# Performance work log

Measured on AMD Instinct MI355X. Metric: run time of the kernel, lower is better.

Reference implementation:

```python
import jax, jax.numpy as jnp
import numpy as np

B, R, C, NH, G = 32, 64, 96, 3, 8   # batch, patches_resolution, dim, heads, group(window) size
HD = C // NH                         # head dim = 32
SCALE = HD ** -0.5
HID = 4 * C                          # mlp hidden = mlp_ratio * dim


def setup_inputs() -> dict:
    key = jax.random.key(0)
    ks = jax.random.split(key, 16)
    n = jax.random.normal
    s = 0.02
    return {
        "x": n(ks[0], (B, R * R, C), jnp.float32),
        "w_qkv": n(ks[1], (C, 3 * C), jnp.float32) * s,
        "b_qkv": jnp.zeros((3 * C,), jnp.float32),
        "w_lepe": n(ks[2], (C, 1, 3, 3), jnp.float32) * s,  # depthwise conv, OIHW with groups=C
        "b_lepe": jnp.zeros((C,), jnp.float32),
        "w_proj": n(ks[3], (C, C), jnp.float32) * s,
        "b_proj": jnp.zeros((C,), jnp.float32),
        "g1": jnp.ones((C,), jnp.float32),
        "bt1": jnp.zeros((C,), jnp.float32),
        "g2": jnp.ones((C,), jnp.float32),
        "bt2": jnp.zeros((C,), jnp.float32),
        "w_fc1": n(ks[4], (C, HID), jnp.float32) * s,
        "b_fc1": jnp.zeros((HID,), jnp.float32),
        "w_fc2": n(ks[5], (HID, C), jnp.float32) * s,
        "b_fc2": jnp.zeros((C,), jnp.float32),
    }


def _ln(x, g, b):
    m = x.mean(-1, keepdims=True)
    v = ((x - m) ** 2).mean(-1, keepdims=True)
    return (x - m) * jax.lax.rsqrt(v + 1e-5) * g + b


def reference(x, w_qkv, b_qkv, w_lepe, b_lepe, w_proj, b_proj,
              g1, bt1, g2, bt2, w_fc1, b_fc1, w_fc2, b_fc2):
    Bn, L, _ = x.shape
    H = W = R
    shortcut = x
    # norm1 + SDA window partition: (B,H,W,C) -> (B*nW, G*G, C)
    h = _ln(x, g1, bt1).reshape(Bn, H // G, G, W // G, G, C)
    h = h.transpose(0, 1, 3, 2, 4, 5).reshape(-1, G * G, C)
    B_ = h.shape[0]
    qkv = (h @ w_qkv + b_qkv).reshape(B_, G * G, 3, NH, HD).transpose(2, 0, 3, 1, 4)
    q, k, v = qkv[0], qkv[1], qkv[2]            # (B_, NH, G*G, HD)
    # LePE: depthwise 3x3 conv on V viewed as (B_, C, G, G)
    vimg = v.transpose(0, 1, 3, 2).reshape(B_, C, G, G)
    lepe = jax.lax.conv_general_dilated(
        vimg, w_lepe, window_strides=(1, 1), padding='SAME',
        feature_group_count=C, dimension_numbers=('NCHW', 'OIHW', 'NCHW'))
    lepe = lepe + b_lepe[None, :, None, None]
    lepe = lepe.reshape(B_, NH, HD, G * G).transpose(0, 1, 3, 2)  # (B_, NH, G*G, HD)
    # attention (no mask registered in this block)
    attn = jax.nn.softmax((q * SCALE) @ k.transpose(0, 1, 3, 2), axis=-1)
    o = (attn @ v + lepe).transpose(0, 2, 1, 3).reshape(B_, G * G, C)
    o = o @ w_proj + b_proj
    # window reverse
    o = o.reshape(Bn, H // G, W // G, G, G, C).transpose(0, 1, 3, 2, 4, 5).reshape(Bn, L, C)
    x1 = shortcut + o
    # MLP block (exact GELU, as torch nn.GELU default)
    m = _ln(x1, g2, bt2)
    m = jax.nn.gelu(m @ w_fc1 + b_fc1, approximate=False) @ w_fc2 + b_fc2
    return (x1 + m, attn)
```

## Files before the change

kernel.cpp:

```cpp
#include <hip/hip_runtime.h>
#include <hip/hip_bf16.h>

typedef short short8 __attribute__((ext_vector_type(8)));
typedef float f32x4 __attribute__((ext_vector_type(4)));

constexpr int BDIM = 32, RDIM = 64, CDIM = 96, NH_ = 3, HD_ = 32;
constexpr int LTOK = RDIM * RDIM;
constexpr int GG = 64;
constexpr int HID = 384;
constexpr int NWIN = 2048;
constexpr float SCALE = 0.17677669529663687f;
constexpr long OUT1OFF = (long)BDIM * LTOK * CDIM;

constexpr int O_WQKVT = 0;
constexpr int O_WPROJT = 27648;
constexpr int O_WFC1T = 36864;
constexpr int O_WFC2T = 73728;
constexpr int W_TOT = 110592;

__device__ __forceinline__ unsigned short f2b(float f) {
  return __builtin_bit_cast(unsigned short, __float2bfloat16(f));
}
__device__ __forceinline__ float b2f(unsigned short u) {
  return __bfloat162float(__builtin_bit_cast(__hip_bfloat16, u));
}

__global__ void prep_weights(const float* __restrict__ wqkv,
                             const float* __restrict__ wproj,
                             const float* __restrict__ wfc1,
                             const float* __restrict__ wfc2,
                             unsigned short* __restrict__ ws) {
  int i = blockIdx.x * 256 + threadIdx.x;
  if (i >= W_TOT) return;
  float v;
  if (i < O_WPROJT) {
    int n = i / 96, k = i - n * 96;
    v = wqkv[k * 288 + n];
  } else if (i < O_WFC1T) {
    int j = i - O_WPROJT, n = j / 96, k = j - n * 96;
    v = wproj[k * 96 + n];
  } else if (i < O_WFC2T) {
    int j = i - O_WFC1T, n = j / 96, k = j - n * 96;
    v = wfc1[k * 384 + n];
  } else {
    int j = i - O_WFC2T, n = j / 384, k = j - n * 384;
    v = wfc2[k * 96 + n];
  }
  ws[i] = f2b(v);
}

__global__ __launch_bounds__(256, 2)
void attn_mfma(const float* __restrict__ x, const float* __restrict__ bqkv,
               const float* __restrict__ wlepe, const float* __restrict__ blepe,
               const float* __restrict__ bproj, const float* __restrict__ g1,
               const float* __restrict__ bt1,
               const unsigned short* __restrict__ ws, float* __restrict__ out) {
  constexpr int SA = 104;
  constexpr int SQ = 200;
  constexpr int SV = 72;
  constexpr int SP = 72;
  __shared__ __attribute__((aligned(16))) unsigned short hA[64 * SA];
  __shared__ __attribute__((aligned(16))) unsigned short qkS[64 * SQ];
  __shared__ __attribute__((aligned(16))) unsigned short vS[96 * SV];
  __shared__ __attribute__((aligned(16))) unsigned short pS[64 * SP];
  float* red = (float*)pS;

  const int tid = threadIdx.x, lane = tid & 63;
  const int wv = __builtin_amdgcn_readfirstlane(tid >> 6);
  const int w = blockIdx.x, b = w >> 6, wi = w & 63, wr = wi >> 3, wc = wi & 7;
  const long xbase = (long)b * (LTOK * CDIM);
  const int l15 = lane & 15, lk = (lane >> 4) * 8, lr = (lane >> 4) * 4;

  {
    const int tok = lane;
    const long rowbase =
        xbase + (long)((wr * 8 + (tok >> 3)) * RDIM + wc * 8 + (tok & 7)) * CDIM;
    float xv[24], s1 = 0.f, s2 = 0.f;
#pragma unroll
    for (int i = 0; i < 24; ++i) {
      float v = x[rowbase + wv * 24 + i];
      xv[i] = v; s1 += v; s2 += v * v;
    }
    red[wv * 64 + tok] = s1;
    red[256 + wv * 64 + tok] = s2;
    __syncthreads();
    float m = 0.f, vv = 0.f;
#pragma unroll
    for (int q = 0; q < 4; ++q) { m += red[q * 64 + tok]; vv += red[256 + q * 64 + tok]; }
    m *= (1.f / 96.f);
    vv = vv * (1.f / 96.f) - m * m;
    float rs = rsqrtf(vv + 1e-5f);
#pragma unroll
    for (int i = 0; i < 24; ++i) {
      int c = wv * 24 + i;
      hA[tok * SA + c] = f2b((xv[i] - m) * rs * g1[c] + bt1[c]);
    }
  }
  __syncthreads();

  {
    f32x4 acc[18];
#pragma unroll
    for (int t = 0; t < 18; ++t) acc[t] = (f32x4){0.f, 0.f, 0.f, 0.f};
    const int arow = wv * 16 + l15;
#pragma unroll
    for (int kk = 0; kk < 3; ++kk) {
      short8 a = *(const short8*)&hA[arow * SA + kk * 32 + lk];
#pragma unroll
      for (int nt = 0; nt < 18; ++nt) {
        short8 bw = *(const short8*)&ws[O_WQKVT + (nt * 16 + l15) * 96 + kk * 32 + lk];
        acc[nt] = __builtin_amdgcn_mfma_f32_16x16x32_bf16(a, bw, acc[nt], 0, 0, 0);
      }
    }
#pragma unroll
    for (int nt = 0; nt < 18; ++nt) {
      int n0 = nt * 16 + l15;
      float bias = bqkv[n0];
#pragma unroll
      for (int r = 0; r < 4; ++r) {
        int tk = wv * 16 + lr + r;
        float v = acc[nt][r] + bias;
        if (n0 < 96) qkS[tk * SQ + n0] = f2b(v * SCALE);
        else if (n0 < 192) qkS[tk * SQ + n0] = f2b(v);
        else vS[(n0 - 192) * SV + tk] = f2b(v);
      }
    }
  }
  __syncthreads();

  for (int h = 0; h < NH_; ++h) {
    f32x4 sacc[4];
#pragma unroll
    for (int t = 0; t < 4; ++t) sacc[t] = (f32x4){0.f, 0.f, 0.f, 0.f};
    short8 aq = *(const short8*)&qkS[(wv * 16 + l15) * SQ + h * 32 + lk];
#pragma unroll
    for (int nt = 0; nt < 4; ++nt) {
      short8 bk = *(const short8*)&qkS[(nt * 16 + l15) * SQ + 96 + h * 32 + lk];
      sacc[nt] = __builtin_amdgcn_mfma_f32_16x16x32_bf16(aq, bk, sacc[nt], 0, 0, 0);
    }
    float p[4][4];
#pragma unroll
    for (int r = 0; r < 4; ++r) {
      float mx = -1e30f;
#pragma unroll
      for (int nt = 0; nt < 4; ++nt) mx = fmaxf(mx, sacc[nt][r]);
#pragma unroll
      for (int s = 1; s < 16; s <<= 1) mx = fmaxf(mx, __shfl_xor(mx, s, 64));
      float sum = 0.f;
#pragma unroll
      for (int nt = 0; nt < 4; ++nt) {
        float e = __expf(sacc[nt][r] - mx);
        p[nt][r] = e; sum += e;
      }
#pragma unroll
      for (int s = 1; s < 16; s <<= 1) sum += __shfl_xor(sum, s, 64);
      float inv = 1.f / sum;
#pragma unroll
      for (int nt = 0; nt < 4; ++nt) p[nt][r] *= inv;
    }
    const long o1base = OUT1OFF + ((long)(w * NH_ + h) * GG) * GG;
#pragma unroll
    for (int nt = 0; nt < 4; ++nt) {
      int col = nt * 16 + l15;
#pragma unroll
      for (int r = 0; r < 4; ++r) {
        int row = wv * 16 + lr + r;
        out[o1base + (long)row * GG + col] = p[nt][r];
        pS[row * SP + col] = f2b(p[nt][r]);
      }
    }
    f32x4 oa[2];
    oa[0] = (f32x4){0.f, 0.f, 0.f, 0.f};
    oa[1] = (f32x4){0.f, 0.f, 0.f, 0.f};
#pragma unroll
    for (int kk = 0; kk < 2; ++kk) {
      short8 ap = *(const short8*)&pS[(wv * 16 + l15) * SP + kk * 32 + lk];
#pragma unroll
      for (int nt = 0; nt < 2; ++nt) {
        short8 bv = *(const short8*)&vS[(h * 32 + nt * 16 + l15) * SV + kk * 32 + lk];
        oa[nt] = __builtin_amdgcn_mfma_f32_16x16x32_bf16(ap, bv, oa[nt], 0, 0, 0);
      }
    }
#pragma unroll
    for (int nt = 0; nt < 2; ++nt) {
      int d = nt * 16 + l15, c = h * 32 + d;
      float lw9[9];
#pragma unroll
      for (int q = 0; q < 9; ++q) lw9[q] = wlepe[c * 9 + q];
      float lb = blepe[c];
#pragma unroll
      for (int r = 0; r < 4; ++r) {
        int tk = wv * 16 + lr + r;
        int tr_ = tk >> 3, tc_ = tk & 7;
        float a = lb;
#pragma unroll
        for (int kh = 0; kh < 3; ++kh)
#pragma unroll
          for (int kw2 = 0; kw2 < 3; ++kw2) {
            int rr = tr_ + kh - 1, cc = tc_ + kw2 - 1;
            if (rr >= 0 && rr < 8 && cc >= 0 && cc < 8)
              a += lw9[kh * 3 + kw2] * b2f(vS[c * SV + rr * 8 + cc]);
          }
        hA[tk * SA + c] = f2b(oa[nt][r] + a);
      }
    }
  }
  __syncthreads();

  {
    f32x4 pacc[6];
#pragma unroll
    for (int t = 0; t < 6; ++t) pacc[t] = (f32x4){0.f, 0.f, 0.f, 0.f};
#pragma unroll
    for (int kk = 0; kk < 3; ++kk) {
      short8 ao = *(const short8*)&hA[(wv * 16 + l15) * SA + kk * 32 + lk];
#pragma unroll
      for (int nt = 0; nt < 6; ++nt) {
        short8 bw = *(const short8*)&ws[O_WPROJT + (nt * 16 + l15) * 96 + kk * 32 + lk];
        pacc[nt] = __builtin_amdgcn_mfma_f32_16x16x32_bf16(ao, bw, pacc[nt], 0, 0, 0);
      }
    }
#pragma unroll
    for (int nt = 0; nt < 6; ++nt) {
      int ch = nt * 16 + l15;
      float bias = bproj[ch];
#pragma unroll
      for (int r = 0; r < 4; ++r) {
        int tk = wv * 16 + lr + r;
        long g = xbase + (long)((wr * 8 + (tk >> 3)) * RDIM + wc * 8 + (tk & 7)) * CDIM + ch;
        out[g] = x[g] + pacc[nt][r] + bias;
      }
    }
  }
}

__global__ __launch_bounds__(256, 2)
void mlp_mfma(const float* __restrict__ bfc1, const float* __restrict__ bfc2,
              const float* __restrict__ g2, const float* __restrict__ bt2,
              const unsigned short* __restrict__ ws, float* __restrict__ out) {
  constexpr int SB = 104, SH = 392;
  __shared__ __attribute__((aligned(16))) unsigned short hB[64 * SB];
  __shared__ __attribute__((aligned(16))) unsigned short Hs[64 * SH];
  float* red = (float*)Hs;

  const int tid = threadIdx.x, lane = tid & 63;
  const int wv = __builtin_amdgcn_readfirstlane(tid >> 6);
  const long t0 = (long)blockIdx.x * GG;
  const int l15 = lane & 15, lk = (lane >> 4) * 8, lr = (lane >> 4) * 4;

  {
    const int tok = lane;
    const long rb = (t0 + tok) * CDIM;
    float xv[24], s1 = 0.f, s2 = 0.f;
#pragma unroll
    for (int i = 0; i < 24; ++i) {
      float v = out[rb + wv * 24 + i];
      xv[i] = v; s1 += v; s2 += v * v;
    }
    red[wv * 64 + tok] = s1;
    red[256 + wv * 64 + tok] = s2;
    __syncthreads();
    float m = 0.f, vv = 0.f;
#pragma unroll
    for (int q = 0; q < 4; ++q) { m += red[q * 64 + tok]; vv += red[256 + q * 64 + tok]; }
    m *= (1.f / 96.f);
    vv = vv * (1.f / 96.f) - m * m;
    float rs = rsqrtf(vv + 1e-5f);
#pragma unroll
    for (int i = 0; i < 24; ++i) {
      int c = wv * 24 + i;
      hB[tok * SB + c] = f2b((xv[i] - m) * rs * g2[c] + bt2[c]);
    }
  }
  __syncthreads();

  for (int half = 0; half < 2; ++half) {
    f32x4 acc[12];
#pragma unroll
    for (int t = 0; t < 12; ++t) acc[t] = (f32x4){0.f, 0.f, 0.f, 0.f};
#pragma unroll
    for (int kk = 0; kk < 3; ++kk) {
      short8 a = *(const short8*)&hB[(wv * 16 + l15) * SB + kk * 32 + lk];
#pragma unroll
      for (int nt = 0; nt < 12; ++nt) {
        int n = half * 192 + nt * 16 + l15;
        short8 bw = *(const short8*)&ws[O_WFC1T + n * 96 + kk * 32 + lk];
        acc[nt] = __builtin_amdgcn_mfma_f32_16x16x32_bf16(a, bw, acc[nt], 0, 0, 0);
      }
    }
#pragma unroll
    for (int nt = 0; nt < 12; ++nt) {
      int n = half * 192 + nt * 16 + l15;
      float bias = bfc1[n];
#pragma unroll
      for (int r = 0; r < 4; ++r) {
        int tk = wv * 16 + lr + r;
        float v = acc[nt][r] + bias;
        float gl = 0.5f * v * (1.f + erff(v * 0.70710678118654752f));
        Hs[tk * SH + n] = f2b(gl);
      }
    }
  }
  __syncthreads();

  {
    f32x4 acc[6];
#pragma unroll
    for (int t = 0; t < 6; ++t) acc[t] = (f32x4){0.f, 0.f, 0.f, 0.f};
#pragma unroll
    for (int kk = 0; kk < 12; ++kk) {
      short8 a = *(const short8*)&Hs[(wv * 16 + l15) * SH + kk * 32 + lk];
#pragma unroll
      for (int nt = 0; nt < 6; ++nt) {
        short8 bw = *(const short8*)&ws[O_WFC2T + (nt * 16 + l15) * 384 + kk * 32 + lk];
        acc[nt] = __builtin_amdgcn_mfma_f32_16x16x32_bf16(a, bw, acc[nt], 0, 0, 0);
      }
    }
#pragma unroll
    for (int nt = 0; nt < 6; ++nt) {
      int ch = nt * 16 + l15;
      float bias = bfc2[ch];
#pragma unroll
      for (int r = 0; r < 4; ++r) {
        int tk = wv * 16 + lr + r;
        long g = (t0 + tk) * CDIM + ch;
        out[g] = out[g] + acc[nt][r] + bias;
      }
    }
  }
}

struct PF {
  const float *x, *w_qkv, *b_qkv, *w_lepe, *b_lepe, *w_proj, *b_proj;
  const float *g1, *bt1, *g2, *bt2, *w_fc1, *b_fc1, *w_fc2, *b_fc2;
  float* out;
};

__global__ __launch_bounds__(256, 2)
void attn_scalar(PF p) {
  constexpr int SA = 66;
  __shared__ __hip_bfloat16 bufA[CDIM * SA];
  __shared__ __hip_bfloat16 qkvT[288 * GG];
  __shared__ __hip_bfloat16 sPad[GG * SA];
  __shared__ float meanS[GG], rstdS[GG];

  const int w = blockIdx.x;
  const int b = w >> 6, wi = w & 63, wr = wi >> 3, wc = wi & 7;
  const int tid = threadIdx.x, lane = tid & 63;
  const int wv = __builtin_amdgcn_readfirstlane(tid >> 6);
  const long xbase = (long)b * (LTOK * CDIM);

  for (int k = 0; k < 24; ++k) {
    int e = tid + k * 256, wrow = e / 768, o = e - wrow * 768;
    int tir = o / 96, ch = o - tir * 96;
    long g = xbase + ((wr * 8 + wrow) * RDIM + wc * 8 + tir) * CDIM + ch;
    bufA[ch * SA + wrow * 8 + tir] = __float2bfloat16(p.x[g]);
  }
  __syncthreads();
  if (wv == 0) {
    float m = 0.f;
    for (int c = 0; c < CDIM; ++c) m += __bfloat162float(bufA[c * SA + lane]);
    m *= (1.f / CDIM);
    float var = 0.f;
    for (int c = 0; c < CDIM; ++c) {
      float d = __bfloat162float(bufA[c * SA + lane]) - m;
      var += d * d;
    }
    meanS[lane] = m;
    rstdS[lane] = rsqrtf(var * (1.f / CDIM) + 1e-5f);
  }
  __syncthreads();
  {
    float m = meanS[lane], rs = rstdS[lane];
    for (int cc = 0; cc < 24; ++cc) {
      int c = wv * 24 + cc;
      float v = __bfloat162float(bufA[c * SA + lane]);
      bufA[c * SA + lane] = __float2bfloat16((v - m) * rs * p.g1[c] + p.bt1[c]);
    }
  }
  __syncthreads();
  for (int tile = 0; tile < 2; ++tile) {
    int j0 = wv * 72 + tile * 36;
    float acc[36];
#pragma unroll
    for (int jj = 0; jj < 36; ++jj) acc[jj] = p.b_qkv[j0 + jj];
#pragma unroll 1
    for (int c = 0; c < CDIM; ++c) {
      float hv = __bfloat162float(bufA[c * SA + lane]);
#pragma unroll
      for (int jj = 0; jj < 36; ++jj) acc[jj] += hv * p.w_qkv[c * 288 + j0 + jj];
    }
#pragma unroll
    for (int jj = 0; jj < 36; ++jj)
      qkvT[(j0 + jj) * GG + lane] = __float2bfloat16(acc[jj]);
  }
  __syncthreads();
  for (int hh = 0; hh < NH_; ++hh) {
    float kreg[HD_];
#pragma unroll
    for (int d = 0; d < HD_; ++d)
      kreg[d] = __bfloat162float(qkvT[(CDIM + hh * HD_ + d) * GG + lane]);
#pragma unroll 1
    for (int r = 0; r < 16; ++r) {
      int i = wv * 16 + r;
      float acc = 0.f;
#pragma unroll
      for (int d = 0; d < HD_; ++d)
        acc += __bfloat162float(qkvT[(hh * HD_ + d) * GG + i]) * kreg[d];
      sPad[lane * SA + i] = __float2bfloat16(acc * SCALE);
    }
#pragma unroll 1
    for (int r = 0; r < 16; ++r) {
      int i = wv * 16 + r;
      float v = __bfloat162float(sPad[lane * SA + i]);
      float mx = v;
#pragma unroll
      for (int s = 32; s > 0; s >>= 1) mx = fmaxf(mx, __shfl_xor(mx, s, 64));
      float e = __expf(v - mx);
      float sum = e;
#pragma unroll
      for (int s = 32; s > 0; s >>= 1) sum += __shfl_xor(sum, s, 64);
      float rr = e / sum;
      sPad[lane * SA + i] = __float2bfloat16(rr);
      p.out[OUT1OFF + ((long)(w * NH_ + hh) * GG + i) * GG + lane] = rr;
    }
    __syncthreads();
    {
      int d0 = wv * 8;
      float acc[8];
#pragma unroll
      for (int dd = 0; dd < 8; ++dd) acc[dd] = 0.f;
#pragma unroll 1
      for (int j = 0; j < GG; ++j) {
        float sv = __bfloat162float(sPad[j * SA + lane]);
#pragma unroll
        for (int dd = 0; dd < 8; ++dd)
          acc[dd] += sv * __bfloat162float(qkvT[(2 * CDIM + hh * HD_ + d0 + dd) * GG + j]);
      }
      int tr = lane >> 3, tc = lane & 7;
#pragma unroll
      for (int dd = 0; dd < 8; ++dd) {
        int c = hh * HD_ + d0 + dd;
        float a = p.b_lepe[c];
#pragma unroll
        for (int kh = 0; kh < 3; ++kh)
#pragma unroll
          for (int kw = 0; kw < 3; ++kw) {
            int rr2 = tr + kh - 1, cc2 = tc + kw - 1;
            if (rr2 >= 0 && rr2 < 8 && cc2 >= 0 && cc2 < 8)
              a += p.w_lepe[c * 9 + kh * 3 + kw] *
                   __bfloat162float(qkvT[(2 * CDIM + hh * HD_ + d0 + dd) * GG + rr2 * 8 + cc2]);
          }
        acc[dd] += a;
      }
#pragma unroll
      for (int dd = 0; dd < 8; ++dd)
        bufA[(hh * HD_ + d0 + dd) * SA + lane] = __float2bfloat16(acc[dd]);
    }
    __syncthreads();
  }
  __hip_bfloat16* projT = qkvT;
  {
    int j0 = wv * 24;
    float acc[24];
#pragma unroll
    for (int jj = 0; jj < 24; ++jj) acc[jj] = p.b_proj[j0 + jj];
#pragma unroll 1
    for (int c = 0; c < CDIM; ++c) {
      float ov = __bfloat162float(bufA[c * SA + lane]);
#pragma unroll
      for (int jj = 0; jj < 24; ++jj) acc[jj] += ov * p.w_proj[c * CDIM + j0 + jj];
    }
#pragma unroll
    for (int jj = 0; jj < 24; ++jj)
      projT[(j0 + jj) * SA + lane] = __float2bfloat16(acc[jj]);
  }
  __syncthreads();
  for (int k = 0; k < 24; ++k) {
    int e = tid + k * 256, wrow = e / 768, o = e - wrow * 768;
    int tir = o / 96, ch = o - tir * 96;
    long g = xbase + ((wr * 8 + wrow) * RDIM + wc * 8 + tir) * CDIM + ch;
    p.out[g] = p.x[g] + __bfloat162float(projT[ch * SA + wrow * 8 + tir]);
  }
}

__global__ __launch_bounds__(256, 2)
void mlp_scalar(PF p) {
  constexpr int SB = 66;
  __shared__ __hip_bfloat16 bufB[CDIM * SB];
  __shared__ __hip_bfloat16 hidT[HID * GG];
  __shared__ float meanS[GG], rstdS[GG];

  const int tid = threadIdx.x, lane = tid & 63;
  const int wv = __builtin_amdgcn_readfirstlane(tid >> 6);
  const long t0 = (long)blockIdx.x * GG;

  for (int k = 0; k < 24; ++k) {
    int e = tid + k * 256, tok = e / 96, ch = e - tok * 96;
    bufB[ch * SB + tok] = __float2bfloat16(p.out[(t0 + tok) * CDIM + ch]);
  }
  __syncthreads();
  if (wv == 0) {
    float m = 0.f;
    for (int c = 0; c < CDIM; ++c) m += __bfloat162float(bufB[c * SB + lane]);
    m *= (1.f / CDIM);
    float var = 0.f;
    for (int c = 0; c < CDIM; ++c) {
      float d = __bfloat162float(bufB[c * SB + lane]) - m;
      var += d * d;
    }
    meanS[lane] = m;
    rstdS[lane] = rsqrtf(var * (1.f / CDIM) + 1e-5f);
  }
  __syncthreads();
  {
    float m = meanS[lane], rs = rstdS[lane];
    for (int cc = 0; cc < 24; ++cc) {
      int c = wv * 24 + cc;
      float v = __bfloat162float(bufB[c * SB + lane]);
      bufB[c * SB + lane] = __float2bfloat16((v - m) * rs * p.g2[c] + p.bt2[c]);
    }
  }
  __syncthreads();
  for (int tile = 0; tile < 4; ++tile) {
    int j0 = wv * 96 + tile * 24;
    float acc[24];
#pragma unroll
    for (int jj = 0; jj < 24; ++jj) acc[jj] = p.b_fc1[j0 + jj];
#pragma unroll 1
    for (int c = 0; c < CDIM; ++c) {
      float hv = __bfloat162float(bufB[c * SB + lane]);
#pragma unroll
      for (int jj = 0; jj < 24; ++jj) acc[jj] += hv * p.w_fc1[c * HID + j0 + jj];
    }
#pragma unroll
    for (int jj = 0; jj < 24; ++jj) {
      float xg = acc[jj];
      hidT[(j0 + jj) * GG + lane] =
          __float2bfloat16(0.5f * xg * (1.f + erff(xg * 0.70710678118f)));
    }
  }
  __syncthreads();
  {
    int j0 = wv * 24;
    float acc[24];
#pragma unroll
    for (int jj = 0; jj < 24; ++jj) acc[jj] = p.b_fc2[j0 + jj];
#pragma unroll 1
    for (int h = 0; h < HID; ++h) {
      float hv = __bfloat162float(hidT[h * GG + lane]);
#pragma unroll
      for (int jj = 0; jj < 24; ++jj) acc[jj] += hv * p.w_fc2[h * CDIM + j0 + jj];
    }
#pragma unroll
    for (int jj = 0; jj < 24; ++jj)
      bufB[(j0 + jj) * SB + lane] = __float2bfloat16(acc[jj]);
  }
  __syncthreads();
  for (int k = 0; k < 24; ++k) {
    int e = tid + k * 256, tok = e / 96, ch = e - tok * 96;
    long g = (t0 + tok) * CDIM + ch;
    p.out[g] = p.out[g] + __bfloat162float(bufB[ch * SB + tok]);
  }
}

extern "C" void kernel_launch(void* const* d_in, const int* in_sizes, int n_in,
                              void* d_out, int out_size, void* d_ws, size_t ws_size,
                              hipStream_t stream) {
  const float* x = (const float*)d_in[0];
  const float* w_qkv = (const float*)d_in[1];
  const float* b_qkv = (const float*)d_in[2];
  const float* w_lepe = (const float*)d_in[3];
  const float* b_lepe = (const float*)d_in[4];
  const float* w_proj = (const float*)d_in[5];
  const float* b_proj = (const float*)d_in[6];
  const float* g1 = (const float*)d_in[7];
  const float* bt1 = (const float*)d_in[8];
  const float* g2 = (const float*)d_in[9];
  const float* bt2 = (const float*)d_in[10];
  const float* w_fc1 = (const float*)d_in[11];
  const float* b_fc1 = (const float*)d_in[12];
  const float* w_fc2 = (const float*)d_in[13];
  const float* b_fc2 = (const float*)d_in[14];
  float* out = (float*)d_out;
  const int mlp_blocks = (BDIM * LTOK) / GG;

  if (ws_size >= (size_t)W_TOT * sizeof(unsigned short)) {
    unsigned short* ws = (unsigned short*)d_ws;
    prep_weights<<<(W_TOT + 255) / 256, 256, 0, stream>>>(w_qkv, w_proj, w_fc1, w_fc2, ws);
    attn_mfma<<<NWIN, 256, 0, stream>>>(x, b_qkv, w_lepe, b_lepe, b_proj, g1, bt1, ws, out);
    mlp_mfma<<<mlp_blocks, 256, 0, stream>>>(b_fc1, b_fc2, g2, bt2, ws, out);
  } else {
    PF p{x, w_qkv, b_qkv, w_lepe, b_lepe, w_proj, b_proj,
         g1, bt1, g2, bt2, w_fc1, b_fc1, w_fc2, b_fc2, out};
    attn_scalar<<<NWIN, 256, 0, stream>>>(p);
    mlp_scalar<<<mlp_blocks, 256, 0, stream>>>(p);
  }
}
```

Before: 425.8 us.

## Fuse attention and MLP into one per-window kernel with head-streamed QKV

Merges the attention and MLP kernels into a single per-window kernel. The post-attention residual x1 stays in registers and LayerNorm2 is computed in-register via lane shuffles, so x1 is no longer written to and re-read from global memory. QKV is now computed per head and the projection is accumulated per head, and the MLP streams the hidden dimension in 64-wide chunks so fc2 accumulates without a full hidden buffer. Together these shrink LDS use enough to raise the occupancy hint from 2 to 4 blocks, at the cost of more barriers per window. The scalar fallback path is removed, so a workspace buffer is now assumed.

```diff
diff --git a/kernel.cpp b/kernel.cpp
--- a/kernel.cpp
+++ b/kernel.cpp
@@ -4,10 +4,9 @@
 typedef short short8 __attribute__((ext_vector_type(8)));
 typedef float f32x4 __attribute__((ext_vector_type(4)));
 
-constexpr int BDIM = 32, RDIM = 64, CDIM = 96, NH_ = 3, HD_ = 32;
+constexpr int BDIM = 32, RDIM = 64, CDIM = 96;
 constexpr int LTOK = RDIM * RDIM;
 constexpr int GG = 64;
-constexpr int HID = 384;
 constexpr int NWIN = 2048;
 constexpr float SCALE = 0.17677669529663687f;
 constexpr long OUT1OFF = (long)BDIM * LTOK * CDIM;
@@ -49,27 +48,31 @@
   ws[i] = f2b(v);
 }
 
-__global__ __launch_bounds__(256, 2)
-void attn_mfma(const float* __restrict__ x, const float* __restrict__ bqkv,
-               const float* __restrict__ wlepe, const float* __restrict__ blepe,
-               const float* __restrict__ bproj, const float* __restrict__ g1,
-               const float* __restrict__ bt1,
-               const unsigned short* __restrict__ ws, float* __restrict__ out) {
+__global__ __launch_bounds__(256, 4)
+void fused_block(const float* __restrict__ x, const float* __restrict__ bqkv,
+                 const float* __restrict__ wlepe, const float* __restrict__ blepe,
+                 const float* __restrict__ bproj, const float* __restrict__ g1,
+                 const float* __restrict__ bt1, const float* __restrict__ g2v,
+                 const float* __restrict__ bt2, const float* __restrict__ bfc1,
+                 const float* __restrict__ bfc2,
+                 const unsigned short* __restrict__ ws, float* __restrict__ out) {
   constexpr int SA = 104;
-  constexpr int SQ = 200;
+  constexpr int SQ = 72;
   constexpr int SV = 72;
   constexpr int SP = 72;
+  constexpr int SO = 32;
   __shared__ __attribute__((aligned(16))) unsigned short hA[64 * SA];
   __shared__ __attribute__((aligned(16))) unsigned short qkS[64 * SQ];
-  __shared__ __attribute__((aligned(16))) unsigned short vS[96 * SV];
+  __shared__ __attribute__((aligned(16))) unsigned short vS[32 * SV];
   __shared__ __attribute__((aligned(16))) unsigned short pS[64 * SP];
+  __shared__ __attribute__((aligned(16))) unsigned short oS[64 * SO];
   float* red = (float*)pS;
 
   const int tid = threadIdx.x, lane = tid & 63;
   const int wv = __builtin_amdgcn_readfirstlane(tid >> 6);
   const int w = blockIdx.x, b = w >> 6, wi = w & 63, wr = wi >> 3, wc = wi & 7;
   const long xbase = (long)b * (LTOK * CDIM);
-  const int l15 = lane & 15, lk = (lane >> 4) * 8, lr = (lane >> 4) * 4;
+  const int l15 = lane & 15, quad = lane >> 4, lk = quad * 8, lr = quad * 4;
 
   {
     const int tok = lane;
@@ -91,51 +94,67 @@
     vv = vv * (1.f / 96.f) - m * m;
     float rs = rsqrtf(vv + 1e-5f);
 #pragma unroll
-    for (int i = 0; i < 24; ++i) {
-      int c = wv * 24 + i;
-      hA[tok * SA + c] = f2b((xv[i] - m) * rs * g1[c] + bt1[c]);
+    for (int j = 0; j < 3; ++j) {
+      short8 hp;
+#pragma unroll
+      for (int e = 0; e < 8; ++e) {
+        int c = wv * 24 + j * 8 + e;
+        ((unsigned short*)&hp)[e] = f2b((xv[j * 8 + e] - m) * rs * g1[c] + bt1[c]);
+      }
+      *(short8*)&hA[lane * SA + wv * 24 + j * 8] = hp;
     }
   }
   __syncthreads();
 
-  {
-    f32x4 acc[18];
-#pragma unroll
-    for (int t = 0; t < 18; ++t) acc[t] = (f32x4){0.f, 0.f, 0.f, 0.f};
-    const int arow = wv * 16 + l15;
+  short8 Afrag[3];
+#pragma unroll
+  for (int kk = 0; kk < 3; ++kk)
+    Afrag[kk] = *(const short8*)&hA[(wv * 16 + l15) * SA + kk * 32 + lk];
+
+  f32x4 accP[6];
+#pragma unroll
+  for (int t = 0; t < 6; ++t) accP[t] = (f32x4){0.f, 0.f, 0.f, 0.f};
+
+#pragma unroll 1
+  for (int h = 0; h < 3; ++h) {
+    f32x4 acc[6];
+#pragma unroll
+    for (int t = 0; t < 6; ++t) acc[t] = (f32x4){0.f, 0.f, 0.f, 0.f};
 #pragma unroll
     for (int kk = 0; kk < 3; ++kk) {
-      short8 a = *(const short8*)&hA[arow * SA + kk * 32 + lk];
-#pragma unroll
-      for (int nt = 0; nt < 18; ++nt) {
-        short8 bw = *(const short8*)&ws[O_WQKVT + (nt * 16 + l15) * 96 + kk * 32 + lk];
-        acc[nt] = __builtin_amdgcn_mfma_f32_16x16x32_bf16(a, bw, acc[nt], 0, 0, 0);
-      }
-    }
-#pragma unroll
-    for (int nt = 0; nt < 18; ++nt) {
-      int n0 = nt * 16 + l15;
-      float bias = bqkv[n0];
+#pragma unroll
+      for (int t = 0; t < 6; ++t) {
+        int n = (t < 2 ? h * 32 + t * 16
+                       : t < 4 ? 96 + h * 32 + (t - 2) * 16
+                               : 192 + h * 32 + (t - 4) * 16) + l15;
+        short8 bw = *(const short8*)&ws[O_WQKVT + n * 96 + kk * 32 + lk];
+        acc[t] = __builtin_amdgcn_mfma_f32_16x16x32_bf16(Afrag[kk], bw, acc[t], 0, 0, 0);
+      }
+    }
+#pragma unroll
+    for (int t = 0; t < 6; ++t) {
+      int n = (t < 2 ? h * 32 + t * 16
+                     : t < 4 ? 96 + h * 32 + (t - 2) * 16
+                             : 192 + h * 32 + (t - 4) * 16) + l15;
+      float bias = bqkv[n];
 #pragma unroll
       for (int r = 0; r < 4; ++r) {
-        int tk = wv * 16 + lr + r;
-        float v = acc[nt][r] + bias;
-        if (n0 < 96) qkS[tk * SQ + n0] = f2b(v * SCALE);
-        else if (n0 < 192) qkS[tk * SQ + n0] = f2b(v);
-        else vS[(n0 - 192) * SV + tk] = f2b(v);
-      }
-    }
-  }
-  __syncthreads();
-
-  for (int h = 0; h < NH_; ++h) {
+        int row = wv * 16 + lr + r;
+        float v = acc[t][r] + bias;
+        if (t < 2) qkS[row * SQ + t * 16 + l15] = f2b(v * SCALE);
+        else if (t < 4) qkS[row * SQ + 32 + (t - 2) * 16 + l15] = f2b(v);
+        else vS[((t - 4) * 16 + l15) * SV + row] = f2b(v);
+      }
+    }
+    __syncthreads();
+
+    short8 aq = *(const short8*)&qkS[(wv * 16 + l15) * SQ + lk];
     f32x4 sacc[4];
 #pragma unroll
     for (int t = 0; t < 4; ++t) sacc[t] = (f32x4){0.f, 0.f, 0.f, 0.f};
-    short8 aq = *(const short8*)&qkS[(wv * 16 + l15) * SQ + h * 32 + lk];
 #pragma unroll
     for (int nt = 0; nt < 4; ++nt) {
-      short8 bk = *(const short8*)&qkS[(nt * 16 + l15) * SQ + 96 + h * 32 + lk];
+      short8 bk = *(const short8*)&qkS[(nt * 16 + l15) * SQ + 32 + lk];
       sacc[nt] = __builtin_amdgcn_mfma_f32_16x16x32_bf16(aq, bk, sacc[nt], 0, 0, 0);
     }
     float p[4][4];
@@ -158,7 +177,7 @@
 #pragma unroll
       for (int nt = 0; nt < 4; ++nt) p[nt][r] *= inv;
     }
-    const long o1base = OUT1OFF + ((long)(w * NH_ + h) * GG) * GG;
+    const long o1base = OUT1OFF + ((long)(w * 3 + h) * GG) * GG;
 #pragma unroll
     for (int nt = 0; nt < 4; ++nt) {
       int col = nt * 16 + l15;
@@ -177,390 +196,137 @@
       short8 ap = *(const short8*)&pS[(wv * 16 + l15) * SP + kk * 32 + lk];
 #pragma unroll
       for (int nt = 0; nt < 2; ++nt) {
-        short8 bv = *(const short8*)&vS[(h * 32 + nt * 16 + l15) * SV + kk * 32 + lk];
+        short8 bv = *(const short8*)&vS[(nt * 16 + l15) * SV + kk * 32 + lk];
         oa[nt] = __builtin_amdgcn_mfma_f32_16x16x32_bf16(ap, bv, oa[nt], 0, 0, 0);
       }
     }
 #pragma unroll
     for (int nt = 0; nt < 2; ++nt) {
-      int d = nt * 16 + l15, c = h * 32 + d;
-      float lw9[9];
-#pragma unroll
-      for (int q = 0; q < 9; ++q) lw9[q] = wlepe[c * 9 + q];
+      int dl = nt * 16 + l15, c = h * 32 + dl;
+      float lw[9];
+#pragma unroll
+      for (int q = 0; q < 9; ++q) lw[q] = wlepe[c * 9 + q];
       float lb = blepe[c];
 #pragma unroll
       for (int r = 0; r < 4; ++r) {
-        int tk = wv * 16 + lr + r;
-        int tr_ = tk >> 3, tc_ = tk & 7;
+        int row = wv * 16 + lr + r;
+        int tr_ = row >> 3, tc_ = row & 7;
         float a = lb;
 #pragma unroll
         for (int kh = 0; kh < 3; ++kh)
 #pragma unroll
-          for (int kw2 = 0; kw2 < 3; ++kw2) {
-            int rr = tr_ + kh - 1, cc = tc_ + kw2 - 1;
+          for (int kw = 0; kw < 3; ++kw) {
+            int rr = tr_ + kh - 1, cc = tc_ + kw - 1;
             if (rr >= 0 && rr < 8 && cc >= 0 && cc < 8)
-              a += lw9[kh * 3 + kw2] * b2f(vS[c * SV + rr * 8 + cc]);
+              a += lw[kh * 3 + kw] * b2f(vS[dl * SV + rr * 8 + cc]);
           }
-        hA[tk * SA + c] = f2b(oa[nt][r] + a);
-      }
-    }
-  }
-  __syncthreads();
-
-  {
-    f32x4 pacc[6];
-#pragma unroll
-    for (int t = 0; t < 6; ++t) pacc[t] = (f32x4){0.f, 0.f, 0.f, 0.f};
+        oS[row * SO + dl] = f2b(oa[nt][r] + a);
+      }
+    }
+    {
+      short8 ao = *(const short8*)&oS[(wv * 16 + l15) * SO + lk];
+#pragma unroll
+      for (int nt = 0; nt < 6; ++nt) {
+        short8 bw = *(const short8*)&ws[O_WPROJT + (nt * 16 + l15) * 96 + h * 32 + lk];
+        accP[nt] = __builtin_amdgcn_mfma_f32_16x16x32_bf16(ao, bw, accP[nt], 0, 0, 0);
+      }
+    }
+    __syncthreads();
+  }
+
+  float x1v[6][4];
+#pragma unroll
+  for (int nt = 0; nt < 6; ++nt) {
+    int ch = nt * 16 + l15;
+    float bias = bproj[ch];
+#pragma unroll
+    for (int r = 0; r < 4; ++r) {
+      int row = wv * 16 + lr + r;
+      long g = xbase + (long)((wr * 8 + (row >> 3)) * RDIM + wc * 8 + (row & 7)) * CDIM + ch;
+      x1v[nt][r] = x[g] + accP[nt][r] + bias;
+    }
+  }
+
+  float mr[4], rsr[4];
+#pragma unroll
+  for (int r = 0; r < 4; ++r) {
+    float s = 0.f, q = 0.f;
+#pragma unroll
+    for (int nt = 0; nt < 6; ++nt) { float v = x1v[nt][r]; s += v; q += v * v; }
+#pragma unroll
+    for (int sh = 1; sh < 16; sh <<= 1) {
+      s += __shfl_xor(s, sh, 64);
+      q += __shfl_xor(q, sh, 64);
+    }
+    float m = s * (1.f / 96.f);
+    float var = q * (1.f / 96.f) - m * m;
+    mr[r] = m; rsr[r] = rsqrtf(var + 1e-5f);
+  }
+#pragma unroll
+  for (int nt = 0; nt < 6; ++nt) {
+    int ch = nt * 16 + l15;
+    float gg = g2v[ch], bb = bt2[ch];
+#pragma unroll
+    for (int r = 0; r < 4; ++r) {
+      int row = wv * 16 + lr + r;
+      hA[row * SA + ch] = f2b((x1v[nt][r] - mr[r]) * rsr[r] * gg + bb);
+    }
+  }
+  short8 A2[3];
+#pragma unroll
+  for (int kk = 0; kk < 3; ++kk)
+    A2[kk] = *(const short8*)&hA[(wv * 16 + l15) * SA + kk * 32 + lk];
+
+  unsigned short* Ht = qkS;
+  f32x4 accF[6];
+#pragma unroll
+  for (int t = 0; t < 6; ++t) accF[t] = (f32x4){0.f, 0.f, 0.f, 0.f};
+#pragma unroll 1
+  for (int ht = 0; ht < 6; ++ht) {
+    f32x4 a1[4];
+#pragma unroll
+    for (int t = 0; t < 4; ++t) a1[t] = (f32x4){0.f, 0.f, 0.f, 0.f};
 #pragma unroll
     for (int kk = 0; kk < 3; ++kk) {
-      short8 ao = *(const short8*)&hA[(wv * 16 + l15) * SA + kk * 32 + lk];
+#pragma unroll
+      for (int nt = 0; nt < 4; ++nt) {
+        int n = ht * 64 + nt * 16 + l15;
+        short8 bw = *(const short8*)&ws[O_WFC1T + n * 96 + kk * 32 + lk];
+        a1[nt] = __builtin_amdgcn_mfma_f32_16x16x32_bf16(A2[kk], bw, a1[nt], 0, 0, 0);
+      }
+    }
+#pragma unroll
+    for (int nt = 0; nt < 4; ++nt) {
+      int n = ht * 64 + nt * 16 + l15;
+      float bias = bfc1[n];
+#pragma unroll
+      for (int r = 0; r < 4; ++r) {
+        float v = a1[nt][r] + bias;
+        float gl = 0.5f * v * (1.f + erff(v * 0.70710678118654752f));
+        Ht[(wv * 16 + lr + r) * SQ + nt * 16 + l15] = f2b(gl);
+      }
+    }
+#pragma unroll
+    for (int kk = 0; kk < 2; ++kk) {
+      short8 ah = *(const short8*)&Ht[(wv * 16 + l15) * SQ + kk * 32 + lk];
 #pragma unroll
       for (int nt = 0; nt < 6; ++nt) {
-        short8 bw = *(const short8*)&ws[O_WPROJT + (nt * 16 + l15) * 96 + kk * 32 + lk];
-        pacc[nt] = __builtin_amdgcn_mfma_f32_16x16x32_bf16(ao, bw, pacc[nt], 0, 0, 0);
-      }
-    }
-#pragma unroll
-    for (int nt = 0; nt < 6; ++nt) {
-      int ch = nt * 16 + l15;
-      float bias = bproj[ch];
-#pragma unroll
-      for (int r = 0; r < 4; ++r) {
-        int tk = wv * 16 + lr + r;
-        long g = xbase + (long)((wr * 8 + (tk >> 3)) * RDIM + wc * 8 + (tk & 7)) * CDIM + ch;
-        out[g] = x[g] + pacc[nt][r] + bias;
-      }
-    }
-  }
-}
-
-__global__ __launch_bounds__(256, 2)
-void mlp_mfma(const float* __restrict__ bfc1, const float* __restrict__ bfc2,
-              const float* __restrict__ g2, const float* __restrict__ bt2,
-              const unsigned short* __restrict__ ws, float* __restrict__ out) {
-  constexpr int SB = 104, SH = 392;
-  __shared__ __attribute__((aligned(16))) unsigned short hB[64 * SB];
-  __shared__ __attribute__((aligned(16))) unsigned short Hs[64 * SH];
-  float* red = (float*)Hs;
-
-  const int tid = threadIdx.x, lane = tid & 63;
-  const int wv = __builtin_amdgcn_readfirstlane(tid >> 6);
-  const long t0 = (long)blockIdx.x * GG;
-  const int l15 = lane & 15, lk = (lane >> 4) * 8, lr = (lane >> 4) * 4;
-
-  {
-    const int tok = lane;
-    const long rb = (t0 + tok) * CDIM;
-    float xv[24], s1 = 0.f, s2 = 0.f;
-#pragma unroll
-    for (int i = 0; i < 24; ++i) {
-      float v = out[rb + wv * 24 + i];
-      xv[i] = v; s1 += v; s2 += v * v;
-    }
-    red[wv * 64 + tok] = s1;
-    red[256 + wv * 64 + tok] = s2;
-    __syncthreads();
-    float m = 0.f, vv = 0.f;
-#pragma unroll
-    for (int q = 0; q < 4; ++q) { m += red[q * 64 + tok]; vv += red[256 + q * 64 + tok]; }
-    m *= (1.f / 96.f);
-    vv = vv * (1.f / 96.f) - m * m;
-    float rs = rsqrtf(vv + 1e-5f);
-#pragma unroll
-    for (int i = 0; i < 24; ++i) {
-      int c = wv * 24 + i;
-      hB[tok * SB + c] = f2b((xv[i] - m) * rs * g2[c] + bt2[c]);
-    }
-  }
-  __syncthreads();
-
-  for (int half = 0; half < 2; ++half) {
-    f32x4 acc[12];
-#pragma unroll
-    for (int t = 0; t < 12; ++t) acc[t] = (f32x4){0.f, 0.f, 0.f, 0.f};
-#pragma unroll
-    for (int kk = 0; kk < 3; ++kk) {
-      short8 a = *(const short8*)&hB[(wv * 16 + l15) * SB + kk * 32 + lk];
-#pragma unroll
-      for (int nt = 0; nt < 12; ++nt) {
-        int n = half * 192 + nt * 16 + l15;
-        short8 bw = *(const short8*)&ws[O_WFC1T + n * 96 + kk * 32 + lk];
-        acc[nt] = __builtin_amdgcn_mfma_f32_16x16x32_bf16(a, bw, acc[nt], 0, 0, 0);
-      }
-    }
-#pragma unroll
-    for (int nt = 0; nt < 12; ++nt) {
-      int n = half * 192 + nt * 16 + l15;
-      float bias = bfc1[n];
-#pragma unroll
-      for (int r = 0; r < 4; ++r) {
-        int tk = wv * 16 + lr + r;
-        float v = acc[nt][r] + bias;
-        float gl = 0.5f * v * (1.f + erff(v * 0.70710678118654752f));
-        Hs[tk * SH + n] = f2b(gl);
-      }
-    }
-  }
-  __syncthreads();
-
-  {
-    f32x4 acc[6];
-#pragma unroll
-    for (int t = 0; t < 6; ++t) acc[t] = (f32x4){0.f, 0.f, 0.f, 0.f};
-#pragma unroll
-    for (int kk = 0; kk < 12; ++kk) {
-      short8 a = *(const short8*)&Hs[(wv * 16 + l15) * SH + kk * 32 + lk];
-#pragma unroll
-      for (int nt = 0; nt < 6; ++nt) {
-        short8 bw = *(const short8*)&ws[O_WFC2T + (nt * 16 + l15) * 384 + kk * 32 + lk];
-        acc[nt] = __builtin_amdgcn_mfma_f32_16x16x32_bf16(a, bw, acc[nt], 0, 0, 0);
-      }
-    }
-#pragma unroll
-    for (int nt = 0; nt < 6; ++nt) {
-      int ch = nt * 16 + l15;
-      float bias = bfc2[ch];
-#pragma unroll
-      for (int r = 0; r < 4; ++r) {
-        int tk = wv * 16 + lr + r;
-        long g = (t0 + tk) * CDIM + ch;
-        out[g] = out[g] + acc[nt][r] + bias;
-      }
-    }
-  }
-}
-
-struct PF {
-  const float *x, *w_qkv, *b_qkv, *w_lepe, *b_lepe, *w_proj, *b_proj;
-  const float *g1, *bt1, *g2, *bt2, *w_fc1, *b_fc1, *w_fc2, *b_fc2;
-  float* out;
-};
-
-__global__ __launch_bounds__(256, 2)
-void attn_scalar(PF p) {
-  constexpr int SA = 66;
-  __shared__ __hip_bfloat16 bufA[CDIM * SA];
-  __shared__ __hip_bfloat16 qkvT[288 * GG];
-  __shared__ __hip_bfloat16 sPad[GG * SA];
-  __shared__ float meanS[GG], rstdS[GG];
-
-  const int w = blockIdx.x;
-  const int b = w >> 6, wi = w & 63, wr = wi >> 3, wc = wi & 7;
-  const int tid = threadIdx.x, lane = tid & 63;
-  const int wv = __builtin_amdgcn_readfirstlane(tid >> 6);
-  const long xbase = (long)b * (LTOK * CDIM);
-
-  for (int k = 0; k < 24; ++k) {
-    int e = tid + k * 256, wrow = e / 768, o = e - wrow * 768;
-    int tir = o / 96, ch = o - tir * 96;
-    long g = xbase + ((wr * 8 + wrow) * RDIM + wc * 8 + tir) * CDIM + ch;
-    bufA[ch * SA + wrow * 8 + tir] = __float2bfloat16(p.x[g]);
-  }
-  __syncthreads();
-  if (wv == 0) {
-    float m = 0.f;
-    for (int c = 0; c < CDIM; ++c) m += __bfloat162float(bufA[c * SA + lane]);
-    m *= (1.f / CDIM);
-    float var = 0.f;
-    for (int c = 0; c < CDIM; ++c) {
-      float d = __bfloat162float(bufA[c * SA + lane]) - m;
-      var += d * d;
-    }
-    meanS[lane] = m;
-    rstdS[lane] = rsqrtf(var * (1.f / CDIM) + 1e-5f);
-  }
-  __syncthreads();
-  {
-    float m = meanS[lane], rs = rstdS[lane];
-    for (int cc = 0; cc < 24; ++cc) {
-      int c = wv * 24 + cc;
-      float v = __bfloat162float(bufA[c * SA + lane]);
-      bufA[c * SA + lane] = __float2bfloat16((v - m) * rs * p.g1[c] + p.bt1[c]);
-    }
-  }
-  __syncthreads();
-  for (int tile = 0; tile < 2; ++tile) {
-    int j0 = wv * 72 + tile * 36;
-    float acc[36];
-#pragma unroll
-    for (int jj = 0; jj < 36; ++jj) acc[jj] = p.b_qkv[j0 + jj];
-#pragma unroll 1
-    for (int c = 0; c < CDIM; ++c) {
-      float hv = __bfloat162float(bufA[c * SA + lane]);
-#pragma unroll
-      for (int jj = 0; jj < 36; ++jj) acc[jj] += hv * p.w_qkv[c * 288 + j0 + jj];
-    }
-#pragma unroll
-    for (int jj = 0; jj < 36; ++jj)
-      qkvT[(j0 + jj) * GG + lane] = __float2bfloat16(acc[jj]);
-  }
-  __syncthreads();
-  for (int hh = 0; hh < NH_; ++hh) {
-    float kreg[HD_];
-#pragma unroll
-    for (int d = 0; d < HD_; ++d)
-      kreg[d] = __bfloat162float(qkvT[(CDIM + hh * HD_ + d) * GG + lane]);
-#pragma unroll 1
-    for (int r = 0; r < 16; ++r) {
-      int i = wv * 16 + r;
-      float acc = 0.f;
-#pragma unroll
-      for (int d = 0; d < HD_; ++d)
-        acc += __bfloat162float(qkvT[(hh * HD_ + d) * GG + i]) * kreg[d];
-      sPad[lane * SA + i] = __float2bfloat16(acc * SCALE);
-    }
-#pragma unroll 1
-    for (int r = 0; r < 16; ++r) {
-      int i = wv * 16 + r;
-      float v = __bfloat162float(sPad[lane * SA + i]);
-      float mx = v;
-#pragma unroll
-      for (int s = 32; s > 0; s >>= 1) mx = fmaxf(mx, __shfl_xor(mx, s, 64));
-      float e = __expf(v - mx);
-      float sum = e;
-#pragma unroll
-      for (int s = 32; s > 0; s >>= 1) sum += __shfl_xor(sum, s, 64);
-      float rr = e / sum;
-      sPad[lane * SA + i] = __float2bfloat16(rr);
-      p.out[OUT1OFF + ((long)(w * NH_ + hh) * GG + i) * GG + lane] = rr;
-    }
-    __syncthreads();
-    {
-      int d0 = wv * 8;
-      float acc[8];
-#pragma unroll
-      for (int dd = 0; dd < 8; ++dd) acc[dd] = 0.f;
-#pragma unroll 1
-      for (int j = 0; j < GG; ++j) {
-        float sv = __bfloat162float(sPad[j * SA + lane]);
-#pragma unroll
-        for (int dd = 0; dd < 8; ++dd)
-          acc[dd] += sv * __bfloat162float(qkvT[(2 * CDIM + hh * HD_ + d0 + dd) * GG + j]);
-      }
-      int tr = lane >> 3, tc = lane & 7;
-#pragma unroll
-      for (int dd = 0; dd < 8; ++dd) {
-        int c = hh * HD_ + d0 + dd;
-        float a = p.b_lepe[c];
-#pragma unroll
-        for (int kh = 0; kh < 3; ++kh)
-#pragma unroll
-          for (int kw = 0; kw < 3; ++kw) {
-            int rr2 = tr + kh - 1, cc2 = tc + kw - 1;
-            if (rr2 >= 0 && rr2 < 8 && cc2 >= 0 && cc2 < 8)
-              a += p.w_lepe[c * 9 + kh * 3 + kw] *
-                   __bfloat162float(qkvT[(2 * CDIM + hh * HD_ + d0 + dd) * GG + rr2 * 8 + cc2]);
-          }
-        acc[dd] += a;
-      }
-#pragma unroll
-      for (int dd = 0; dd < 8; ++dd)
-        bufA[(hh * HD_ + d0 + dd) * SA + lane] = __float2bfloat16(acc[dd]);
-    }
-    __syncthreads();
-  }
-  __hip_bfloat16* projT = qkvT;
-  {
-    int j0 = wv * 24;
-    float acc[24];
-#pragma unroll
-    for (int jj = 0; jj < 24; ++jj) acc[jj] = p.b_proj[j0 + jj];
-#pragma unroll 1
-    for (int c = 0; c < CDIM; ++c) {
-      float ov = __bfloat162float(bufA[c * SA + lane]);
-#pragma unroll
-      for (int jj = 0; jj < 24; ++jj) acc[jj] += ov * p.w_proj[c * CDIM + j0 + jj];
-    }
-#pragma unroll
-    for (int jj = 0; jj < 24; ++jj)
-      projT[(j0 + jj) * SA + lane] = __float2bfloat16(acc[jj]);
-  }
-  __syncthreads();
-  for (int k = 0; k < 24; ++k) {
-    int e = tid + k * 256, wrow = e / 768, o = e - wrow * 768;
-    int tir = o / 96, ch = o - tir * 96;
-    long g = xbase + ((wr * 8 + wrow) * RDIM + wc * 8 + tir) * CDIM + ch;
-    p.out[g] = p.x[g] + __bfloat162float(projT[ch * SA + wrow * 8 + tir]);
-  }
-}
-
-__global__ __launch_bounds__(256, 2)
-void mlp_scalar(PF p) {
-  constexpr int SB = 66;
-  __shared__ __hip_bfloat16 bufB[CDIM * SB];
-  __shared__ __hip_bfloat16 hidT[HID * GG];
-  __shared__ float meanS[GG], rstdS[GG];
-
-  const int tid = threadIdx.x, lane = tid & 63;
-  const int wv = __builtin_amdgcn_readfirstlane(tid >> 6);
-  const long t0 = (long)blockIdx.x * GG;
-
-  for (int k = 0; k < 24; ++k) {
-    int e = tid + k * 256, tok = e / 96, ch = e - tok * 96;
-    bufB[ch * SB + tok] = __float2bfloat16(p.out[(t0 + tok) * CDIM + ch]);
-  }
-  __syncthreads();
-  if (wv == 0) {
-    float m = 0.f;
-    for (int c = 0; c < CDIM; ++c) m += __bfloat162float(bufB[c * SB + lane]);
-    m *= (1.f / CDIM);
-    float var = 0.f;
-    for (int c = 0; c < CDIM; ++c) {
-      float d = __bfloat162float(bufB[c * SB + lane]) - m;
-      var += d * d;
-    }
-    meanS[lane] = m;
-    rstdS[lane] = rsqrtf(var * (1.f / CDIM) + 1e-5f);
-  }
-  __syncthreads();
-  {
-    float m = meanS[lane], rs = rstdS[lane];
-    for (int cc = 0; cc < 24; ++cc) {
-      int c = wv * 24 + cc;
-      float v = __bfloat162float(bufB[c * SB + lane]);
-      bufB[c * SB + lane] = __float2bfloat16((v - m) * rs * p.g2[c] + p.bt2[c]);
-    }
-  }
-  __syncthreads();
-  for (int tile = 0; tile < 4; ++tile) {
-    int j0 = wv * 96 + tile * 24;
-    float acc[24];
-#pragma unroll
-    for (int jj = 0; jj < 24; ++jj) acc[jj] = p.b_fc1[j0 + jj];
-#pragma unroll 1
-    for (int c = 0; c < CDIM; ++c) {
-      float hv = __bfloat162float(bufB[c * SB + lane]);
-#pragma unroll
-      for (int jj = 0; jj < 24; ++jj) acc[jj] += hv * p.w_fc1[c * HID + j0 + jj];
-    }
-#pragma unroll
-    for (int jj = 0; jj < 24; ++jj) {
-      float xg = acc[jj];
-      hidT[(j0 + jj) * GG + lane] =
-          __float2bfloat16(0.5f * xg * (1.f + erff(xg * 0.70710678118f)));
-    }
-  }
-  __syncthreads();
-  {
-    int j0 = wv * 24;
-    float acc[24];
-#pragma unroll
-    for (int jj = 0; jj < 24; ++jj) acc[jj] = p.b_fc2[j0 + jj];
-#pragma unroll 1
-    for (int h = 0; h < HID; ++h) {
-      float hv = __bfloat162float(hidT[h * GG + lane]);
-#pragma unroll
-      for (int jj = 0; jj < 24; ++jj) acc[jj] += hv * p.w_fc2[h * CDIM + j0 + jj];
-    }
-#pragma unroll
-    for (int jj = 0; jj < 24; ++jj)
-      bufB[(j0 + jj) * SB + lane] = __float2bfloat16(acc[jj]);
-  }
-  __syncthreads();
-  for (int k = 0; k < 24; ++k) {
-    int e = tid + k * 256, tok = e / 96, ch = e - tok * 96;
-    long g = (t0 + tok) * CDIM + ch;
-    p.out[g] = p.out[g] + __bfloat162float(bufB[ch * SB + tok]);
+        short8 bw = *(const short8*)&ws[O_WFC2T + (nt * 16 + l15) * 384 + ht * 64 + kk * 32 + lk];
+        accF[nt] = __builtin_amdgcn_mfma_f32_16x16x32_bf16(ah, bw, accF[nt], 0, 0, 0);
+      }
+    }
+  }
+
+#pragma unroll
+  for (int nt = 0; nt < 6; ++nt) {
+    int ch = nt * 16 + l15;
+    float bias = bfc2[ch];
+#pragma unroll
+    for (int r = 0; r < 4; ++r) {
+      int row = wv * 16 + lr + r;
+      long g = xbase + (long)((wr * 8 + (row >> 3)) * RDIM + wc * 8 + (row & 7)) * CDIM + ch;
+      out[g] = x1v[nt][r] + accF[nt][r] + bias;
+    }
   }
 }
 
@@ -583,17 +349,9 @@
   const float* w_fc2 = (const float*)d_in[13];
   const float* b_fc2 = (const float*)d_in[14];
   float* out = (float*)d_out;
-  const int mlp_blocks = (BDIM * LTOK) / GG;
-
-  if (ws_size >= (size_t)W_TOT * sizeof(unsigned short)) {
-    unsigned short* ws = (unsigned short*)d_ws;
-    prep_weights<<<(W_TOT + 255) / 256, 256, 0, stream>>>(w_qkv, w_proj, w_fc1, w_fc2, ws);
-    attn_mfma<<<NWIN, 256, 0, stream>>>(x, b_qkv, w_lepe, b_lepe, b_proj, g1, bt1, ws, out);
-    mlp_mfma<<<mlp_blocks, 256, 0, stream>>>(b_fc1, b_fc2, g2, bt2, ws, out);
-  } else {
-    PF p{x, w_qkv, b_qkv, w_lepe, b_lepe, w_proj, b_proj,
-         g1, bt1, g2, bt2, w_fc1, b_fc1, w_fc2, b_fc2, out};
-    attn_scalar<<<NWIN, 256, 0, stream>>>(p);
-    mlp_scalar<<<mlp_blocks, 256, 0, stream>>>(p);
-  }
-}
+  unsigned short* ws = (unsigned short*)d_ws;
+
+  prep_weights<<<(W_TOT + 255) / 256, 256, 0, stream>>>(w_qkv, w_proj, w_fc1, w_fc2, ws);
+  fused_block<<<NWIN, 256, 0, stream>>>(x, b_qkv, w_lepe, b_lepe, b_proj, g1, bt1,
+                                        g2, bt2, b_fc1, b_fc2, ws, out);
+}
```

After: 453.0 us. 6.4% more time.
